# Kernel optimization log

Hardware: AMD Instinct MI355X
Metric: run time of the kernel (lower is better)

## Reference

```python
import jax, jax.numpy as jnp
import numpy as np

N_NODES = 50000


def _gcn_norm(edge_index, num_nodes):
    # Add self-loops, compute symmetric normalization D^-1/2 (A+I) D^-1/2
    loops = jnp.arange(num_nodes, dtype=edge_index.dtype)
    row = jnp.concatenate([edge_index[0], loops])  # source
    col = jnp.concatenate([edge_index[1], loops])  # target
    deg = jax.ops.segment_sum(jnp.ones_like(col, dtype=jnp.float32), col,
                              num_segments=num_nodes)
    dinv = jnp.where(deg > 0, jax.lax.rsqrt(deg), 0.0)
    norm = dinv[row] * dinv[col]  # [E + N]
    return row, col, norm


def _gcn_conv(x, W, b, row, col, norm, num_nodes):
    h = x @ W                              # [N, F_out] small GEMM first (as in PyG)
    msg = h[row] * norm[:, None]           # gather + scale  [E+N, F_out]
    out = jax.ops.segment_sum(msg, col, num_segments=num_nodes)  # scatter-add
    return out + b


def setup_inputs() -> dict:
    key = jax.random.key(0)
    k = jax.random.split(key, 6)
    enc_in, hidden = 128, 16
    x = jax.random.normal(k[0], (N_NODES, enc_in), dtype=jnp.float32)
    edge_index = jax.random.randint(k[1], (2, 600000), 0, N_NODES, dtype=jnp.int64)
    # Glorot-ish init for weights
    W1 = jax.random.normal(k[2], (enc_in, hidden), dtype=jnp.float32) * (1.0 / np.sqrt(enc_in))
    b1 = jnp.zeros((hidden,), dtype=jnp.float32)
    W2 = jax.random.normal(k[3], (hidden, enc_in), dtype=jnp.float32) * (1.0 / np.sqrt(hidden))
    b2 = jnp.zeros((enc_in,), dtype=jnp.float32)
    return {"x": x, "edge_index": edge_index, "W1": W1, "b1": b1, "W2": W2, "b2": b2}


def reference(x, edge_index, W1, b1, W2, b2):
    row, col, norm = _gcn_norm(edge_index, N_NODES)
    h = _gcn_conv(x, W1, b1, row, col, norm, N_NODES)
    h = jax.nn.relu(h)
    # dropout is identity in eval mode
    h = _gcn_conv(h, W2, b2, row, col, norm, N_NODES)
    return jax.nn.log_softmax(h, axis=1)
```

## Files before the change

### kernel.cpp

```cpp
#include <hip/hip_runtime.h>

#define NN 50000
#define FIN 128
#define FH 16
#define CAP 64

__global__ void k_build(const int* __restrict__ row, const int* __restrict__ col,
                        int* __restrict__ cnt, int* __restrict__ slot, int E) {
    int e = blockIdx.x * blockDim.x + threadIdx.x;
    if (e >= E) return;
    int r = row[e], c = col[e];
    int pos = atomicAdd(&cnt[c], 1);
    if (pos < CAP) slot[c * CAP + pos] = r;
}

__global__ __launch_bounds__(256) void k_gemm1(const float* __restrict__ x,
                                               const float* __restrict__ W1,
                                               const int* __restrict__ cnt,
                                               float* __restrict__ dinv,
                                               float* __restrict__ g1, int n) {
    int i = blockIdx.x * blockDim.x + threadIdx.x;
    if (i >= n) return;
    float acc[FH];
#pragma unroll
    for (int j = 0; j < FH; ++j) acc[j] = 0.f;
    const float4* xr = (const float4*)(x + (size_t)i * FIN);
#pragma unroll 4
    for (int kk = 0; kk < FIN / 4; ++kk) {
        float4 xv = xr[kk];
        const float* w = W1 + kk * 4 * FH;
#pragma unroll
        for (int j = 0; j < FH; ++j)
            acc[j] += xv.x * w[j] + xv.y * w[FH + j] + xv.z * w[2 * FH + j] + xv.w * w[3 * FH + j];
    }
    float d = rsqrtf((float)cnt[i] + 1.0f);
    dinv[i] = d;
    float4* o = (float4*)(g1 + (size_t)i * FH);
#pragma unroll
    for (int q = 0; q < 4; ++q)
        o[q] = make_float4(acc[4 * q] * d, acc[4 * q + 1] * d, acc[4 * q + 2] * d, acc[4 * q + 3] * d);
}

__global__ __launch_bounds__(256) void k_agg1(const float* __restrict__ g1,
                                              const int* __restrict__ cnt,
                                              const int* __restrict__ slot,
                                              const float* __restrict__ dinv,
                                              const float* __restrict__ b1,
                                              float* __restrict__ g2, int n4) {
    int gid = blockIdx.x * blockDim.x + threadIdx.x;
    if (gid >= n4) return;
    int i = gid >> 2, q = gid & 3;
    float4 s = ((const float4*)g1)[gid];
    int d = cnt[i];
    if (d > CAP) d = CAP;
    const int* sl = slot + i * CAP;
    int e = 0;
    for (; e + 4 <= d; e += 4) {
        int r0 = sl[e], r1 = sl[e + 1], r2 = sl[e + 2], r3 = sl[e + 3];
        float4 a0 = ((const float4*)g1)[r0 * 4 + q];
        float4 a1 = ((const float4*)g1)[r1 * 4 + q];
        float4 a2 = ((const float4*)g1)[r2 * 4 + q];
        float4 a3 = ((const float4*)g1)[r3 * 4 + q];
        s.x += (a0.x + a1.x) + (a2.x + a3.x);
        s.y += (a0.y + a1.y) + (a2.y + a3.y);
        s.z += (a0.z + a1.z) + (a2.z + a3.z);
        s.w += (a0.w + a1.w) + (a2.w + a3.w);
    }
    for (; e < d; ++e) {
        float4 a = ((const float4*)g1)[sl[e] * 4 + q];
        s.x += a.x; s.y += a.y; s.z += a.z; s.w += a.w;
    }
    float di = dinv[i];
    const float* bb = b1 + q * 4;
    float4 o;
    o.x = fmaxf(s.x * di + bb[0], 0.f) * di;
    o.y = fmaxf(s.y * di + bb[1], 0.f) * di;
    o.z = fmaxf(s.z * di + bb[2], 0.f) * di;
    o.w = fmaxf(s.w * di + bb[3], 0.f) * di;
    ((float4*)g2)[gid] = o;
}

__global__ __launch_bounds__(256) void k_agg2final(const float* __restrict__ g2,
                                                   const int* __restrict__ cnt,
                                                   const int* __restrict__ slot,
                                                   const float* __restrict__ dinv,
                                                   const float* __restrict__ W2,
                                                   const float* __restrict__ b2,
                                                   float* __restrict__ out, int n) {
    int wave = threadIdx.x >> 6, lane = threadIdx.x & 63;
    int nd = blockIdx.x * 4 + wave;
    if (nd >= n) return;
    int f = lane & 15, grp = lane >> 4;
    int d = cnt[nd];
    if (d > CAP) d = CAP;
    const int* sl = slot + nd * CAP;
    float p = 0.f;
    for (int e = grp; e < d; e += 4) {
        int r = sl[e];
        p += g2[r * FH + f];
    }
    p += __shfl_xor(p, 16);
    p += __shfl_xor(p, 32);
    p += g2[nd * FH + f];
    p *= dinv[nd];
    float vv[FH];
#pragma unroll
    for (int k = 0; k < FH; ++k) vv[k] = __shfl(p, k);
    float y0 = b2[lane], y1 = b2[lane + 64];
#pragma unroll
    for (int k = 0; k < FH; ++k) {
        y0 += vv[k] * W2[k * FIN + lane];
        y1 += vv[k] * W2[k * FIN + 64 + lane];
    }
    float m = fmaxf(y0, y1);
#pragma unroll
    for (int o = 32; o; o >>= 1) m = fmaxf(m, __shfl_xor(m, o));
    float s = __expf(y0 - m) + __expf(y1 - m);
#pragma unroll
    for (int o = 32; o; o >>= 1) s += __shfl_xor(s, o);
    float ls = m + logf(s);
    out[(size_t)nd * FIN + lane] = y0 - ls;
    out[(size_t)nd * FIN + 64 + lane] = y1 - ls;
}

extern "C" void kernel_launch(void* const* d_in, const int* in_sizes, int n_in,
                              void* d_out, int out_size, void* d_ws, size_t ws_size,
                              hipStream_t stream) {
    const float* x  = (const float*)d_in[0];
    const int*   ei = (const int*)d_in[1];
    const float* W1 = (const float*)d_in[2];
    const float* b1 = (const float*)d_in[3];
    const float* W2 = (const float*)d_in[4];
    const float* b2 = (const float*)d_in[5];
    float* out = (float*)d_out;

    const int N = NN;
    const int E = in_sizes[1] / 2;
    const int* row = ei;
    const int* col = ei + E;

    int*   cnt  = (int*)d_ws;
    float* dinv = (float*)d_ws + 50000;
    float* g1   = (float*)d_ws + 100000;
    float* g2   = (float*)d_ws + 900000;
    int*   slot = (int*)d_ws + 1700000;

    hipMemsetAsync(cnt, 0, N * sizeof(int), stream);
    hipLaunchKernelGGL(k_build, dim3((E + 255) / 256), dim3(256), 0, stream, row, col, cnt, slot, E);
    hipLaunchKernelGGL(k_gemm1, dim3((N + 255) / 256), dim3(256), 0, stream, x, W1, cnt, dinv, g1, N);
    hipLaunchKernelGGL(k_agg1, dim3((N * 4 + 255) / 256), dim3(256), 0, stream, g1, cnt, slot, dinv, b1, g2, N * 4);
    hipLaunchKernelGGL(k_agg2final, dim3((N + 3) / 4), dim3(256), 0, stream, g2, cnt, slot, dinv, W2, b2, out, N);
}
```

Before: 170.0 us.

## Fuse all GCN stages into one cooperative persistent kernel with grid syncs

```diff
diff --git a/kernel.cpp b/kernel.cpp
--- a/kernel.cpp
+++ b/kernel.cpp
@@ -1,9 +1,129 @@
 #include <hip/hip_runtime.h>
+#include <hip/hip_cooperative_groups.h>
+
+namespace cg = cooperative_groups;
 
 #define NN 50000
 #define FIN 128
 #define FH 16
 #define CAP 64
+#define NBLK 512
+#define NTHR 256
+
+__global__ __launch_bounds__(NTHR, 2) void k_fused(
+    const float* __restrict__ x, const int* __restrict__ eidx,
+    const float* __restrict__ W1, const float* __restrict__ b1,
+    const float* __restrict__ W2, const float* __restrict__ b2,
+    int* __restrict__ cnt, int* __restrict__ slot,
+    float* __restrict__ dinv, float* __restrict__ g1, float* __restrict__ g2,
+    float* __restrict__ out, int N, int E)
+{
+    cg::grid_group grid = cg::this_grid();
+    const int tid = blockIdx.x * blockDim.x + threadIdx.x;
+    const int nthreads = NBLK * NTHR;
+    const int* row = eidx;
+    const int* col = eidx + E;
+
+    for (int e = tid; e < E; e += nthreads) {
+        int r = row[e], c = col[e];
+        int pos = atomicAdd(&cnt[c], 1);
+        if (pos < CAP) slot[c * CAP + pos] = r;
+    }
+    grid.sync();
+
+    for (int i = tid; i < N; i += nthreads) {
+        float acc[FH];
+#pragma unroll
+        for (int j = 0; j < FH; ++j) acc[j] = 0.f;
+        const float4* xr = (const float4*)(x + (size_t)i * FIN);
+#pragma unroll 4
+        for (int kk = 0; kk < FIN / 4; ++kk) {
+            float4 xv = xr[kk];
+            const float* w = W1 + kk * 4 * FH;
+#pragma unroll
+            for (int j = 0; j < FH; ++j)
+                acc[j] += xv.x * w[j] + xv.y * w[FH + j] + xv.z * w[2 * FH + j] + xv.w * w[3 * FH + j];
+        }
+        float d = rsqrtf((float)cnt[i] + 1.0f);
+        dinv[i] = d;
+        float4* o = (float4*)(g1 + (size_t)i * FH);
+#pragma unroll
+        for (int q = 0; q < 4; ++q)
+            o[q] = make_float4(acc[4 * q] * d, acc[4 * q + 1] * d, acc[4 * q + 2] * d, acc[4 * q + 3] * d);
+    }
+    grid.sync();
+
+    for (int gid = tid; gid < N * 4; gid += nthreads) {
+        int i = gid >> 2, q = gid & 3;
+        float4 s = ((const float4*)g1)[gid];
+        int d = cnt[i];
+        if (d > CAP) d = CAP;
+        const int* sl = slot + i * CAP;
+        int e = 0;
+        for (; e + 4 <= d; e += 4) {
+            int r0 = sl[e], r1 = sl[e + 1], r2 = sl[e + 2], r3 = sl[e + 3];
+            float4 a0 = ((const float4*)g1)[r0 * 4 + q];
+            float4 a1 = ((const float4*)g1)[r1 * 4 + q];
+            float4 a2 = ((const float4*)g1)[r2 * 4 + q];
+            float4 a3 = ((const float4*)g1)[r3 * 4 + q];
+            s.x += (a0.x + a1.x) + (a2.x + a3.x);
+            s.y += (a0.y + a1.y) + (a2.y + a3.y);
+            s.z += (a0.z + a1.z) + (a2.z + a3.z);
+            s.w += (a0.w + a1.w) + (a2.w + a3.w);
+        }
+        for (; e < d; ++e) {
+            float4 a = ((const float4*)g1)[sl[e] * 4 + q];
+            s.x += a.x; s.y += a.y; s.z += a.z; s.w += a.w;
+        }
+        float di = dinv[i];
+        const float* bb = b1 + q * 4;
+        float4 o;
+        o.x = fmaxf(s.x * di + bb[0], 0.f) * di;
+        o.y = fmaxf(s.y * di + bb[1], 0.f) * di;
+        o.z = fmaxf(s.z * di + bb[2], 0.f) * di;
+        o.w = fmaxf(s.w * di + bb[3], 0.f) * di;
+        ((float4*)g2)[gid] = o;
+    }
+    grid.sync();
+
+    {
+        const int wave = tid >> 6, lane = tid & 63;
+        const int nwaves = nthreads >> 6;
+        const int f = lane & 15, grp = lane >> 4;
+        for (int nd = wave; nd < N; nd += nwaves) {
+            int d = cnt[nd];
+            if (d > CAP) d = CAP;
+            const int* sl = slot + nd * CAP;
+            float p = 0.f;
+            for (int e = grp; e < d; e += 4) {
+                int r = sl[e];
+                p += g2[r * FH + f];
+            }
+            p += __shfl_xor(p, 16);
+            p += __shfl_xor(p, 32);
+            p += g2[nd * FH + f];
+            p *= dinv[nd];
+            float vv[FH];
+#pragma unroll
+            for (int k = 0; k < FH; ++k) vv[k] = __shfl(p, k);
+            float y0 = b2[lane], y1 = b2[lane + 64];
+#pragma unroll
+            for (int k = 0; k < FH; ++k) {
+                y0 += vv[k] * W2[k * FIN + lane];
+                y1 += vv[k] * W2[k * FIN + 64 + lane];
+            }
+            float m = fmaxf(y0, y1);
+#pragma unroll
+            for (int o = 32; o; o >>= 1) m = fmaxf(m, __shfl_xor(m, o));
+            float s = __expf(y0 - m) + __expf(y1 - m);
+#pragma unroll
+            for (int o = 32; o; o >>= 1) s += __shfl_xor(s, o);
+            float ls = m + logf(s);
+            out[(size_t)nd * FIN + lane] = y0 - ls;
+            out[(size_t)nd * FIN + 64 + lane] = y1 - ls;
+        }
+    }
+}
 
 __global__ void k_build(const int* __restrict__ row, const int* __restrict__ col,
                         int* __restrict__ cnt, int* __restrict__ slot, int E) {
@@ -134,10 +254,8 @@
     const float* b2 = (const float*)d_in[5];
     float* out = (float*)d_out;
 
-    const int N = NN;
-    const int E = in_sizes[1] / 2;
-    const int* row = ei;
-    const int* col = ei + E;
+    int N = NN;
+    int E = in_sizes[1] / 2;
 
     int*   cnt  = (int*)d_ws;
     float* dinv = (float*)d_ws + 50000;
@@ -146,8 +264,18 @@
     int*   slot = (int*)d_ws + 1700000;
 
     hipMemsetAsync(cnt, 0, N * sizeof(int), stream);
-    hipLaunchKernelGGL(k_build, dim3((E + 255) / 256), dim3(256), 0, stream, row, col, cnt, slot, E);
-    hipLaunchKernelGGL(k_gemm1, dim3((N + 255) / 256), dim3(256), 0, stream, x, W1, cnt, dinv, g1, N);
-    hipLaunchKernelGGL(k_agg1, dim3((N * 4 + 255) / 256), dim3(256), 0, stream, g1, cnt, slot, dinv, b1, g2, N * 4);
-    hipLaunchKernelGGL(k_agg2final, dim3((N + 3) / 4), dim3(256), 0, stream, g2, cnt, slot, dinv, W2, b2, out, N);
-}
+
+    void* args[] = {(void*)&x, (void*)&ei, (void*)&W1, (void*)&b1, (void*)&W2, (void*)&b2,
+                    (void*)&cnt, (void*)&slot, (void*)&dinv, (void*)&g1, (void*)&g2,
+                    (void*)&out, (void*)&N, (void*)&E};
+    hipError_t err = hipLaunchCooperativeKernel((void*)k_fused, dim3(NBLK), dim3(NTHR),
+                                                args, 0, stream);
+    if (err != hipSuccess) {
+        const int* row = ei;
+        const int* col = ei + E;
+        hipLaunchKernelGGL(k_build, dim3((E + 255) / 256), dim3(256), 0, stream, row, col, cnt, slot, E);
+        hipLaunchKernelGGL(k_gemm1, dim3((N + 255) / 256), dim3(256), 0, stream, x, W1, cnt, dinv, g1, N);
+        hipLaunchKernelGGL(k_agg1, dim3((N * 4 + 255) / 256), dim3(256), 0, stream, g1, cnt, slot, dinv, b1, g2, N * 4);
+        hipLaunchKernelGGL(k_agg2final, dim3((N + 3) / 4), dim3(256), 0, stream, g2, cnt, slot, dinv, W2, b2, out, N);
+    }
+}
```

Result: slower. 420.7 us (+147.5%).

## Merge edge build and GEMM1 into one kernel, shrink slot indices to ushort

Applied to the files above, without the earlier changes.

```diff
diff --git a/kernel.cpp b/kernel.cpp
--- a/kernel.cpp
+++ b/kernel.cpp
@@ -5,72 +5,83 @@
 #define FH 16
 #define CAP 64
 
-__global__ void k_build(const int* __restrict__ row, const int* __restrict__ col,
-                        int* __restrict__ cnt, int* __restrict__ slot, int E) {
-    int e = blockIdx.x * blockDim.x + threadIdx.x;
-    if (e >= E) return;
-    int r = row[e], c = col[e];
-    int pos = atomicAdd(&cnt[c], 1);
-    if (pos < CAP) slot[c * CAP + pos] = r;
-}
-
-__global__ __launch_bounds__(256) void k_gemm1(const float* __restrict__ x,
-                                               const float* __restrict__ W1,
-                                               const int* __restrict__ cnt,
-                                               float* __restrict__ dinv,
-                                               float* __restrict__ g1, int n) {
-    int i = blockIdx.x * blockDim.x + threadIdx.x;
-    if (i >= n) return;
-    float acc[FH];
+#define GEMM_BLKS 196
+#define BUILD_BLKS 1024
+__global__ __launch_bounds__(256) void k_build_gemm(
+    const float* __restrict__ x, const float* __restrict__ W1,
+    const int* __restrict__ row, const int* __restrict__ col,
+    int* __restrict__ cnt, ushort* __restrict__ slot,
+    float* __restrict__ g1, int N, int E)
+{
+    if (blockIdx.x < GEMM_BLKS) {
+        int i = blockIdx.x * blockDim.x + threadIdx.x;
+        if (i >= N) return;
+        float acc[FH];
 #pragma unroll
-    for (int j = 0; j < FH; ++j) acc[j] = 0.f;
-    const float4* xr = (const float4*)(x + (size_t)i * FIN);
+        for (int j = 0; j < FH; ++j) acc[j] = 0.f;
+        const float4* xr = (const float4*)(x + (size_t)i * FIN);
 #pragma unroll 4
-    for (int kk = 0; kk < FIN / 4; ++kk) {
-        float4 xv = xr[kk];
-        const float* w = W1 + kk * 4 * FH;
+        for (int kk = 0; kk < FIN / 4; ++kk) {
+            float4 xv = xr[kk];
+            const float* w = W1 + kk * 4 * FH;
 #pragma unroll
-        for (int j = 0; j < FH; ++j)
-            acc[j] += xv.x * w[j] + xv.y * w[FH + j] + xv.z * w[2 * FH + j] + xv.w * w[3 * FH + j];
+            for (int j = 0; j < FH; ++j)
+                acc[j] += xv.x * w[j] + xv.y * w[FH + j] + xv.z * w[2 * FH + j] + xv.w * w[3 * FH + j];
+        }
+        float4* o = (float4*)(g1 + (size_t)i * FH);
+#pragma unroll
+        for (int q = 0; q < 4; ++q)
+            o[q] = make_float4(acc[4 * q], acc[4 * q + 1], acc[4 * q + 2], acc[4 * q + 3]);
+    } else {
+        int t = (blockIdx.x - GEMM_BLKS) * blockDim.x + threadIdx.x;
+        const int stride = BUILD_BLKS * 256;
+        for (int e = t; e < E; e += stride) {
+            int r = row[e], c = col[e];
+            int pos = atomicAdd(&cnt[c], 1);
+            if (pos < CAP) slot[c * CAP + pos] = (ushort)r;
+        }
     }
-    float d = rsqrtf((float)cnt[i] + 1.0f);
-    dinv[i] = d;
-    float4* o = (float4*)(g1 + (size_t)i * FH);
-#pragma unroll
-    for (int q = 0; q < 4; ++q)
-        o[q] = make_float4(acc[4 * q] * d, acc[4 * q + 1] * d, acc[4 * q + 2] * d, acc[4 * q + 3] * d);
 }
 
 __global__ __launch_bounds__(256) void k_agg1(const float* __restrict__ g1,
                                               const int* __restrict__ cnt,
-                                              const int* __restrict__ slot,
-                                              const float* __restrict__ dinv,
+                                              const ushort* __restrict__ slot,
                                               const float* __restrict__ b1,
+                                              float* __restrict__ dinv,
                                               float* __restrict__ g2, int n4) {
     int gid = blockIdx.x * blockDim.x + threadIdx.x;
     if (gid >= n4) return;
     int i = gid >> 2, q = gid & 3;
-    float4 s = ((const float4*)g1)[gid];
     int d = cnt[i];
+    float di = rsqrtf((float)d + 1.0f);
     if (d > CAP) d = CAP;
-    const int* sl = slot + i * CAP;
+    float4 sv = ((const float4*)g1)[gid];
+    float4 s = make_float4(sv.x * di, sv.y * di, sv.z * di, sv.w * di);
+    const ushort* sl = slot + (size_t)i * CAP;
     int e = 0;
     for (; e + 4 <= d; e += 4) {
-        int r0 = sl[e], r1 = sl[e + 1], r2 = sl[e + 2], r3 = sl[e + 3];
+        ushort4 rr = ((const ushort4*)sl)[e >> 2];
+        int r0 = rr.x, r1 = rr.y, r2 = rr.z, r3 = rr.w;
+        float d0 = rsqrtf((float)cnt[r0] + 1.0f);
+        float d1 = rsqrtf((float)cnt[r1] + 1.0f);
+        float d2 = rsqrtf((float)cnt[r2] + 1.0f);
+        float d3 = rsqrtf((float)cnt[r3] + 1.0f);
         float4 a0 = ((const float4*)g1)[r0 * 4 + q];
         float4 a1 = ((const float4*)g1)[r1 * 4 + q];
         float4 a2 = ((const float4*)g1)[r2 * 4 + q];
         float4 a3 = ((const float4*)g1)[r3 * 4 + q];
-        s.x += (a0.x + a1.x) + (a2.x + a3.x);
-        s.y += (a0.y + a1.y) + (a2.y + a3.y);
-        s.z += (a0.z + a1.z) + (a2.z + a3.z);
-        s.w += (a0.w + a1.w) + (a2.w + a3.w);
+        s.x += a0.x * d0 + a1.x * d1 + a2.x * d2 + a3.x * d3;
+        s.y += a0.y * d0 + a1.y * d1 + a2.y * d2 + a3.y * d3;
+        s.z += a0.z * d0 + a1.z * d1 + a2.z * d2 + a3.z * d3;
+        s.w += a0.w * d0 + a1.w * d1 + a2.w * d2 + a3.w * d3;
     }
     for (; e < d; ++e) {
-        float4 a = ((const float4*)g1)[sl[e] * 4 + q];
-        s.x += a.x; s.y += a.y; s.z += a.z; s.w += a.w;
+        int r = sl[e];
+        float dr = rsqrtf((float)cnt[r] + 1.0f);
+        float4 a = ((const float4*)g1)[r * 4 + q];
+        s.x += a.x * dr; s.y += a.y * dr; s.z += a.z * dr; s.w += a.w * dr;
     }
-    float di = dinv[i];
+    if (q == 0) dinv[i] = di;
     const float* bb = b1 + q * 4;
     float4 o;
     o.x = fmaxf(s.x * di + bb[0], 0.f) * di;
@@ -82,7 +93,7 @@
 
 __global__ __launch_bounds__(256) void k_agg2final(const float* __restrict__ g2,
                                                    const int* __restrict__ cnt,
-                                                   const int* __restrict__ slot,
+                                                   const ushort* __restrict__ slot,
                                                    const float* __restrict__ dinv,
                                                    const float* __restrict__ W2,
                                                    const float* __restrict__ b2,
@@ -93,7 +104,7 @@
     int f = lane & 15, grp = lane >> 4;
     int d = cnt[nd];
     if (d > CAP) d = CAP;
-    const int* sl = slot + nd * CAP;
+    const ushort* sl = slot + (size_t)nd * CAP;
     float p = 0.f;
     for (int e = grp; e < d; e += 4) {
         int r = sl[e];
@@ -134,20 +145,22 @@
     const float* b2 = (const float*)d_in[5];
     float* out = (float*)d_out;
 
-    const int N = NN;
-    const int E = in_sizes[1] / 2;
+    int N = NN;
+    int E = in_sizes[1] / 2;
     const int* row = ei;
     const int* col = ei + E;
 
-    int*   cnt  = (int*)d_ws;
-    float* dinv = (float*)d_ws + 50000;
-    float* g1   = (float*)d_ws + 100000;
-    float* g2   = (float*)d_ws + 900000;
-    int*   slot = (int*)d_ws + 1700000;
+    int*    cnt  = (int*)d_ws;
+    float*  dinv = (float*)d_ws + 50000;
+    float*  g1   = (float*)d_ws + 100000;
+    float*  g2   = (float*)d_ws + 900000;
+    ushort* slot = (ushort*)((int*)d_ws + 1700000);
 
     hipMemsetAsync(cnt, 0, N * sizeof(int), stream);
-    hipLaunchKernelGGL(k_build, dim3((E + 255) / 256), dim3(256), 0, stream, row, col, cnt, slot, E);
-    hipLaunchKernelGGL(k_gemm1, dim3((N + 255) / 256), dim3(256), 0, stream, x, W1, cnt, dinv, g1, N);
-    hipLaunchKernelGGL(k_agg1, dim3((N * 4 + 255) / 256), dim3(256), 0, stream, g1, cnt, slot, dinv, b1, g2, N * 4);
-    hipLaunchKernelGGL(k_agg2final, dim3((N + 3) / 4), dim3(256), 0, stream, g2, cnt, slot, dinv, W2, b2, out, N);
+    hipLaunchKernelGGL(k_build_gemm, dim3(GEMM_BLKS + BUILD_BLKS), dim3(256), 0, stream,
+                       x, W1, row, col, cnt, slot, g1, N, E);
+    hipLaunchKernelGGL(k_agg1, dim3((N * 4 + 255) / 256), dim3(256), 0, stream,
+                       g1, cnt, slot, b1, dinv, g2, N * 4);
+    hipLaunchKernelGGL(k_agg2final, dim3((N + 3) / 4), dim3(256), 0, stream,
+                       g2, cnt, slot, dinv, W2, b2, out, N);
 }
```

Measured after the change: 161.6 us. 4.9% less time.
